# Kernel tuning notes

Hardware: AMD Instinct MI355X
Metric: run time of the kernel (lower is better)

## Reference

```python
import jax, jax.numpy as jnp
import numpy as np

B, C, N = 2, 128, 4096
BN_EPS = 1e-5


def setup_inputs() -> dict:
    key = jax.random.key(0)
    ks = jax.random.split(key, 16)
    Ch, Cd = C // 2, C // 8

    def bn_params(k1, c):
        k1, k2 = jax.random.split(k1)
        return (1.0 + 0.1 * jax.random.normal(k1, (c,), jnp.float32),  # gamma
                0.1 * jax.random.normal(k2, (c,), jnp.float32),        # beta
                jnp.zeros((c,), jnp.float32),                          # running mean
                jnp.ones((c,), jnp.float32))                           # running var

    g1, be1, m1, v1 = bn_params(ks[4], Ch)
    g2, be2, m2, v2 = bn_params(ks[5], Ch)
    gu, beu, mu, vu = bn_params(ks[6], C)
    return {
        "xyz": jax.random.normal(ks[0], (B, 3, N), jnp.float32),
        "features": jax.random.normal(ks[1], (B, C, N), jnp.float32),
        "w_mlp1": 0.1 * jax.random.normal(ks[2], (Ch, 6), jnp.float32),
        "b_mlp1": jnp.zeros((Ch,), jnp.float32),
        "g_mlp1": g1, "be_mlp1": be1, "m_mlp1": m1, "v_mlp1": v1,
        "w_mlp2": 0.05 * jax.random.normal(ks[3], (Ch, 2 * C), jnp.float32),
        "b_mlp2": jnp.zeros((Ch,), jnp.float32),
        "g_mlp2": g2, "be_mlp2": be2, "m_mlp2": m2, "v_mlp2": v2,
        "w_down1": 0.1 * jax.random.normal(ks[7], (Cd, C), jnp.float32),
        "w_down2": 0.1 * jax.random.normal(ks[8], (Cd, C), jnp.float32),
        "w_up": 0.1 * jax.random.normal(ks[9], (C, Cd), jnp.float32),
        "b_up": jnp.zeros((C,), jnp.float32),
        "g_up": gu, "be_up": beu, "m_up": mu, "v_up": vu,
        "k": 20,
    }


def _knn_idx(x, k):
    # x: [B,3,N]; pairwise_distance = -||xi-xj||^2, topk -> nearest
    xx = jnp.sum(x * x, axis=1)                       # [B,N]
    inner = jnp.einsum('bcn,bcm->bnm', x, x)          # [B,N,N]
    pd = 2.0 * inner - xx[:, :, None] - xx[:, None, :]
    return jax.lax.top_k(pd, k)[1]                    # [B,N,k]


def _gather_edge(feat_t, idx):
    # feat_t: [B,N,C], idx: [B,N,k] -> concat(nbr - center, center): [B,N,k,2C]
    nbr = jax.vmap(lambda a, i: a[i])(feat_t, idx)    # [B,N,k,C]
    center = feat_t[:, :, None, :]
    center_b = jnp.broadcast_to(center, nbr.shape)
    return jnp.concatenate((nbr - center, center_b), axis=-1)


def _bn(x, g, b, m, v, ch_axis=1):
    shape = [1] * x.ndim
    shape[ch_axis] = -1
    r = lambda p: p.reshape(shape)
    return (x - r(m)) * (r(g) / jnp.sqrt(r(v) + BN_EPS)) + r(b)


def reference(xyz, features, w_mlp1, b_mlp1, g_mlp1, be_mlp1, m_mlp1, v_mlp1,
              w_mlp2, b_mlp2, g_mlp2, be_mlp2, m_mlp2, v_mlp2,
              w_down1, w_down2, w_up, b_up, g_up, be_up, m_up, v_up, k):
    idx = _knn_idx(xyz, k)
    edge_x = _gather_edge(jnp.swapaxes(xyz, 1, 2), idx)        # [B,N,k,6]
    edge_f = _gather_edge(jnp.swapaxes(features, 1, 2), idx)   # [B,N,k,2C]

    # 1x1 conv2d + BN + ReLU on both branches (channels last via einsum)
    h1 = jnp.einsum('bnkc,oc->bonk', edge_x, w_mlp1) + b_mlp1[None, :, None, None]
    h1 = jax.nn.relu(_bn(h1, g_mlp1, be_mlp1, m_mlp1, v_mlp1))
    h2 = jnp.einsum('bnkc,oc->bonk', edge_f, w_mlp2) + b_mlp2[None, :, None, None]
    h2 = jax.nn.relu(_bn(h2, g_mlp2, be_mlp2, m_mlp2, v_mlp2))

    f_enc = jnp.max(jnp.concatenate((h1, h2), axis=1), axis=-1)  # [B,C,N]

    f1 = jax.nn.relu(jnp.einsum('bcn,oc->bon', f_enc, w_down1))  # [B,C/8,N]
    f2 = jax.nn.relu(jnp.einsum('bcn,oc->bon', f_enc, w_down2))

    # NOTE: original code indexes [0] after mean -> uses batch element 0 only
    f_channel = jnp.mean(f1, axis=-1, keepdims=True)[0]          # [C/8,1]
    f_space = jnp.mean(f2, axis=1, keepdims=True)[0]             # [1,N]
    final = jnp.sqrt(f_channel @ f_space + 1e-12)                # [C/8,N]
    final = final[None] + f1 + f2                                # [B,C/8,N]

    up = jnp.einsum('bcn,oc->bon', final, w_up) + b_up[None, :, None]
    final = jax.nn.relu(_bn(up, g_up, be_up, m_up, v_up))        # [B,C,N]

    f_local = f_enc - final
    return f_local * jnp.tanh(jax.nn.softplus(f_local))          # Mish
```

## Files before the change

kernel.cpp:

```cpp
#include <hip/hip_runtime.h>
#include <hip/hip_bf16.h>

#define BB 2
#define CC 128
#define NN 4096
#define KK 20

#define WS_FLAG   0
#define WS_FCACC  16
#define WS_S1     32
#define WS_C1     96
#define WS_S2     160
#define WS_C2     224
#define WS_SUP    288
#define WS_CUP    416
#define WS_FS     1024
#define WS_X      8192
#define WS_XX     32768
#define WS_W1     40960
#define WS_W2     41344
#define WS_WD1    57728
#define WS_WD2    59776
#define WS_WUP    61824
#define WS_P      65536
#define WS_Q      1114112
#define WS_FE     2326528
#define WS_F      WS_FE
#define WS_F12    3375104

struct InPtrs { const void* p[22]; };

__device__ __forceinline__ int detect_bf16(const void* xyz) {
  const unsigned* u = (const unsigned*)xyz;
  int cnt = 0;
  for (int i = 0; i < 64; ++i) {
    unsigned lo = u[i] & 0x7FFFu;
    cnt += (lo >= 0x3C00u && lo <= 0x4100u) ? 1 : 0;
  }
  return cnt >= 32;
}

__device__ __forceinline__ float ldin(const void* p, long long i, int flag) {
  if (flag) {
    unsigned short b = ((const unsigned short*)p)[i];
    return __uint_as_float(((unsigned)b) << 16);
  }
  return ((const float*)p)[i];
}

__device__ __forceinline__ double dkey(float v, int m) {
  unsigned u = __float_as_uint(v);
  u = (u & 0x80000000u) ? ~u : (u | 0x80000000u);
  return (double)u * 4096.0 + (double)((NN - 1) - m);
}

__device__ __forceinline__ void insert4d(double key,
    double& a0, double& a1, double& a2, double& a3) {
  bool b0 = key > a0, b1 = key > a1, b2 = key > a2, b3 = key > a3;
  a3 = b3 ? (b2 ? a2 : key) : a3;
  a2 = b2 ? (b1 ? a1 : key) : a2;
  a1 = b1 ? (b0 ? a0 : key) : a1;
  a0 = b0 ? key : a0;
}

__global__ __launch_bounds__(256) void k0_convert(InPtrs in, float* ws) {
  int flag = detect_bf16(in.p[0]);
  int gid = blockIdx.x * 256 + threadIdx.x;
  int stride = gridDim.x * 256;
  if (flag) {
    const ushort4* src = (const ushort4*)in.p[1];
    float4* dst = (float4*)(ws + WS_F);
    for (int i = gid; i < 262144; i += stride) {
      ushort4 s = src[i];
      dst[i] = make_float4(
        __uint_as_float(((unsigned)s.x) << 16), __uint_as_float(((unsigned)s.y) << 16),
        __uint_as_float(((unsigned)s.z) << 16), __uint_as_float(((unsigned)s.w) << 16));
    }
  } else {
    const float4* src = (const float4*)in.p[1];
    float4* dst = (float4*)(ws + WS_F);
    for (int i = gid; i < 262144; i += stride) dst[i] = src[i];
  }
  const int T0 = 24576;
  const int T1 = T0 + 384;
  const int T2 = T1 + 16384;
  const int T3 = T2 + 2048;
  const int T4 = T3 + 2048;
  const int T5 = T4 + 2048;
  for (int i = gid; i < T5; i += stride) {
    const void* src; int off, dst;
    if      (i < T0) { src = in.p[0];  off = i;      dst = WS_X   + off; }
    else if (i < T1) { src = in.p[2];  off = i - T0; dst = WS_W1  + off; }
    else if (i < T2) { src = in.p[8];  off = i - T1; dst = WS_W2  + off; }
    else if (i < T3) { src = in.p[14]; off = i - T2; dst = WS_WD1 + off; }
    else if (i < T4) { src = in.p[15]; off = i - T3; dst = WS_WD2 + off; }
    else             { src = in.p[16]; off = i - T4; dst = WS_WUP + off; }
    ws[dst] = ldin(src, off, flag);
  }
  if (blockIdx.x == 0) {
    int t = threadIdx.x;
    if (t < 64) {
      float b1 = ldin(in.p[3], t, flag), g1 = ldin(in.p[4], t, flag);
      float be1 = ldin(in.p[5], t, flag), m1 = ldin(in.p[6], t, flag), v1 = ldin(in.p[7], t, flag);
      float s1 = g1 / sqrtf(v1 + 1e-5f);
      ws[WS_S1 + t] = s1;
      ws[WS_C1 + t] = s1 * (b1 - m1) + be1;
      float b2 = ldin(in.p[9], t, flag), g2 = ldin(in.p[10], t, flag);
      float be2 = ldin(in.p[11], t, flag), m2 = ldin(in.p[12], t, flag), v2 = ldin(in.p[13], t, flag);
      float s2 = g2 / sqrtf(v2 + 1e-5f);
      ws[WS_S2 + t] = s2;
      ws[WS_C2 + t] = s2 * (b2 - m2) + be2;
    }
    if (t < 128) {
      float bu = ldin(in.p[17], t, flag), gu = ldin(in.p[18], t, flag);
      float beu = ldin(in.p[19], t, flag), mu = ldin(in.p[20], t, flag), vu = ldin(in.p[21], t, flag);
      float su = gu / sqrtf(vu + 1e-5f);
      ws[WS_SUP + t] = su;
      ws[WS_CUP + t] = su * (bu - mu) + beu;
    }
    if (t < 16) ws[WS_FCACC + t] = 0.f;
    if (t == 0) ((int*)ws)[WS_FLAG] = flag;
  }
}

__global__ __launch_bounds__(256) void k1_pq(float* ws) {
  __shared__ float ldsW[64 * 128];
  __shared__ float ldsF[64 * 32];
  int t = threadIdx.x;
  int bid = blockIdx.x;
  int b = bid >> 7;
  int m0 = (bid & 127) << 5;
  int w = t >> 6, sub = (t >> 5) & 1, mloc = t & 31;
  const float* F = ws + WS_F + (long long)b * CC * NN;
  const float* W2 = ws + WS_W2;
  float accP[8], accQ[8];
#pragma unroll
  for (int j = 0; j < 8; ++j) { accP[j] = 0.f; accQ[j] = 0.f; }
  for (int half = 0; half < 2; ++half) {
    if (half) __syncthreads();
    for (int i = t; i < 64 * 128; i += 256) {
      int o = i >> 7, r = i & 127;
      int c = (r & 63) + half * 64 + ((r >> 6) << 7);
      ldsW[i] = W2[o * 256 + c];
    }
    for (int i = t; i < 64 * 32; i += 256) {
      int cl = i >> 5, ml = i & 31;
      ldsF[i] = F[(long long)(half * 64 + cl) * NN + m0 + ml];
    }
    __syncthreads();
    for (int cl = 0; cl < 64; ++cl) {
      float f = ldsF[cl * 32 + mloc];
#pragma unroll
      for (int j = 0; j < 8; ++j) {
        int o = w * 16 + sub * 8 + j;
        accP[j] = fmaf(ldsW[o * 128 + cl], f, accP[j]);
        accQ[j] = fmaf(ldsW[o * 128 + 64 + cl], f, accQ[j]);
      }
    }
  }
  int m = m0 + mloc;
  const float* X = ws + WS_X + (long long)b * 3 * NN;
  float x0 = X[m], x1 = X[NN + m], x2 = X[2 * NN + m];
  const float* W1 = ws + WS_W1;
  float* P = ws + WS_P + ((long long)(b * NN + m)) * 128;
  float* Q = ws + WS_Q + ((long long)(b * NN + m)) * 128;
#pragma unroll
  for (int j = 0; j < 8; ++j) {
    int o = w * 16 + sub * 8 + j;
    float s1 = ws[WS_S1 + o], c1 = ws[WS_C1 + o];
    float px = fmaf(W1[o * 6 + 2], x2, fmaf(W1[o * 6 + 1], x1, W1[o * 6 + 0] * x0));
    float qx = fmaf(W1[o * 6 + 5], x2, fmaf(W1[o * 6 + 4], x1, W1[o * 6 + 3] * x0));
    P[o] = s1 * px;
    Q[o] = fmaf(s1, qx - px, c1);
    float s2 = ws[WS_S2 + o], c2 = ws[WS_C2 + o];
    P[64 + o] = s2 * accP[j];
    Q[64 + o] = fmaf(s2, accQ[j] - accP[j], c2);
  }
  if (t < 32) {
    float xx = __fadd_rn(__fadd_rn(__fmul_rn(x0, x0), __fmul_rn(x1, x1)), __fmul_rn(x2, x2));
    ws[WS_XX + b * NN + m] = xx;
  }
}

__global__ __launch_bounds__(256) void k23_knn_fenc(float* ws) {
  int t = threadIdx.x;
  int w = t >> 6, lane = t & 63;
  int pt = blockIdx.x * 4 + w;
  int b = pt >> 12;
  int n = pt & (NN - 1);
  const float* X = ws + WS_X + (long long)b * 3 * NN;
  const float* XX = ws + WS_XX + (long long)b * NN;
  float xc0 = X[n], xc1 = X[NN + n], xc2 = X[2 * NN + n], xxn = XX[n];
  double a0 = -1.0, a1 = -1.0, a2 = -1.0, a3 = -1.0;
#pragma unroll 4
  for (int s = 0; s < 64; ++s) {
    int m = s * 64 + lane;
    float c0 = X[m], c1 = X[NN + m], c2 = X[2 * NN + m], xxm = XX[m];
    float inner = __fadd_rn(__fadd_rn(__fmul_rn(c0, xc0), __fmul_rn(c1, xc1)), __fmul_rn(c2, xc2));
    float pd = __fsub_rn(__fsub_rn(__fmul_rn(2.0f, inner), xxn), xxm);
    insert4d(dkey(pd, m), a0, a1, a2, a3);
  }
  unsigned long long used = 0;
  int nv = 4;
  double winner = 0.0;
  for (int r = 0; r < KK; ++r) {
    double v = a0;
#pragma unroll
    for (int off = 1; off < 64; off <<= 1)
      v = fmax(v, __shfl_xor(v, off));
    if (lane == r) winner = v;
    if (a0 == v) {
      unsigned hi = (unsigned)(v * (1.0 / 4096.0));
      double rem = v - 4096.0 * (double)hi;
      int mm = (NN - 1) - (int)rem;
      used |= 1ull << (mm >> 6);
      a0 = a1; a1 = a2; a2 = a3; a3 = -1.0; --nv;
      if (nv == 0) {
        a0 = a1 = a2 = a3 = -1.0;
#pragma unroll 1
        for (int s = 0; s < 64; ++s) {
          if (!((used >> s) & 1ull)) {
            int m = s * 64 + lane;
            float c0 = X[m], c1 = X[NN + m], c2 = X[2 * NN + m], xxm = XX[m];
            float inner = __fadd_rn(__fadd_rn(__fmul_rn(c0, xc0), __fmul_rn(c1, xc1)), __fmul_rn(c2, xc2));
            float pd = __fsub_rn(__fsub_rn(__fmul_rn(2.0f, inner), xxn), xxm);
            insert4d(dkey(pd, m), a0, a1, a2, a3);
          }
        }
        nv = 4;
      }
    }
  }
  int myidx;
  {
    unsigned hi = (unsigned)(winner * (1.0 / 4096.0));
    double rem = winner - 4096.0 * (double)hi;
    myidx = (NN - 1) - (int)rem;
  }
  const float* Q = ws + WS_Q + (long long)pt * 128;
  const float* Pb = ws + WS_P + (long long)b * NN * 128;
  float2 q = ((const float2*)Q)[lane];
  float mx0 = -3.4e38f, mx1 = -3.4e38f;
#pragma unroll
  for (int j = 0; j < KK; ++j) {
    int id = __shfl(myidx, j);
    float2 p = ((const float2*)(Pb + (long long)id * 128))[lane];
    mx0 = fmaxf(mx0, p.x + q.x);
    mx1 = fmaxf(mx1, p.y + q.y);
  }
  float2 fe = make_float2(fmaxf(mx0, 0.f), fmaxf(mx1, 0.f));
  ((float2*)(ws + WS_FE + (long long)pt * 128))[lane] = fe;
}

__global__ __launch_bounds__(256) void k4_down(float* ws) {
  __shared__ float ldsFE[8 * 128];
  __shared__ float ldsW[32 * 129];
  __shared__ float ldsFC[16];
  int t = threadIdx.x;
  int b = blockIdx.x >> 9;
  int n0 = (blockIdx.x & 511) << 3;
  for (int i = t; i < 8 * 128; i += 256) {
    int p = i >> 7, c = i & 127;
    ldsFE[i] = ws[WS_FE + (long long)(b * NN + n0 + p) * 128 + c];
  }
  for (int i = t; i < 32 * 128; i += 256) {
    int o = i >> 7, c = i & 127;
    ldsW[o * 129 + c] = (o < 16) ? ws[WS_WD1 + o * 128 + c] : ws[WS_WD2 + (o - 16) * 128 + c];
  }
  if (t < 16) ldsFC[t] = 0.f;
  __syncthreads();
  int p = t >> 5, oid = t & 31;
  float acc = 0.f;
#pragma unroll 8
  for (int c = 0; c < 128; ++c)
    acc = fmaf(ldsW[oid * 129 + c], ldsFE[p * 128 + c], acc);
  float v = fmaxf(acc, 0.f);
  ws[WS_F12 + (long long)(b * NN + n0 + p) * 32 + oid] = v;
  if (b == 0) {
    if (oid >= 16) {
      float s = v;
#pragma unroll
      for (int d = 1; d < 16; d <<= 1) s += __shfl_xor(s, d);
      if (oid == 16) ws[WS_FS + n0 + p] = s * 0.0625f;
    } else {
      atomicAdd(&ldsFC[oid], v);
    }
  }
  __syncthreads();
  if (b == 0 && t < 16) atomicAdd(ws + WS_FCACC + t, ldsFC[t]);
}

__global__ __launch_bounds__(256) void k5_final(float* ws, float* outf, __hip_bfloat16* outb) {
  __shared__ float fin[16 * 16];
  int t = threadIdx.x;
  int g = t >> 4;
  int p = t & 15;
  int b = blockIdx.x >> 8;
  int n0 = (blockIdx.x & 255) << 4;
  int n = n0 + p;
  int flag = ((const int*)ws)[WS_FLAG];
  {
    float fs = ws[WS_FS + n];
    float fc = ws[WS_FCACC + g] * (1.0f / NN);
    float f1v = ws[WS_F12 + (long long)(b * NN + n) * 32 + g];
    float f2v = ws[WS_F12 + (long long)(b * NN + n) * 32 + 16 + g];
    fin[p * 16 + g] = sqrtf(fc * fs + 1e-12f) + f1v + f2v;
  }
  __syncthreads();
  const float4* FE4 = (const float4*)(ws + WS_FE + (long long)(b * NN + n) * 128 + g * 8);
  float fev[8];
  {
    float4 a = FE4[0], c = FE4[1];
    fev[0] = a.x; fev[1] = a.y; fev[2] = a.z; fev[3] = a.w;
    fev[4] = c.x; fev[5] = c.y; fev[6] = c.z; fev[7] = c.w;
  }
#pragma unroll
  for (int j = 0; j < 8; ++j) {
    int o = g * 8 + j;
    float acc = 0.f;
#pragma unroll
    for (int c = 0; c < 16; ++c)
      acc = fmaf(ws[WS_WUP + o * 16 + c], fin[p * 16 + c], acc);
    float fo = fmaf(ws[WS_SUP + o], acc, ws[WS_CUP + o]);
    fo = fmaxf(fo, 0.f);
    float fl = fev[j] - fo;
    float u = __expf(fl);
    float nmr = u * (u + 2.f);
    float y = fl * __fdividef(nmr, nmr + 2.f);
    if (fl > 15.f) y = fl;
    long long oi = ((long long)b * CC + o) * NN + n;
    if (flag) outb[oi] = __float2bfloat16(y);
    else      outf[oi] = y;
  }
}

extern "C" void kernel_launch(void* const* d_in, const int* in_sizes, int n_in,
                              void* d_out, int out_size, void* d_ws, size_t ws_size,
                              hipStream_t stream) {
  (void)in_sizes; (void)out_size; (void)ws_size;
  float* ws = (float*)d_ws;
  InPtrs ip;
  for (int i = 0; i < 22; ++i) ip.p[i] = (i < n_in) ? d_in[i] : nullptr;
  hipLaunchKernelGGL(k0_convert,   dim3(512),          dim3(256), 0, stream, ip, ws);
  hipLaunchKernelGGL(k1_pq,        dim3(256),          dim3(256), 0, stream, ws);
  hipLaunchKernelGGL(k23_knn_fenc, dim3(BB * NN / 4),  dim3(256), 0, stream, ws);
  hipLaunchKernelGGL(k4_down,      dim3(BB * NN / 8),  dim3(256), 0, stream, ws);
  hipLaunchKernelGGL(k5_final,     dim3(BB * NN / 16), dim3(256), 0, stream, ws,
                     (float*)d_out, (__hip_bfloat16*)d_out);
}
```

Measured before the change: 224.2 us.

## Fuse input conversion into consumers and merge down-projection into KNN kernel

```diff
diff --git a/kernel.cpp b/kernel.cpp
--- a/kernel.cpp
+++ b/kernel.cpp
@@ -6,26 +6,13 @@
 #define NN 4096
 #define KK 20
 
-#define WS_FLAG   0
 #define WS_FCACC  16
-#define WS_S1     32
-#define WS_C1     96
-#define WS_S2     160
-#define WS_C2     224
-#define WS_SUP    288
-#define WS_CUP    416
 #define WS_FS     1024
 #define WS_X      8192
 #define WS_XX     32768
-#define WS_W1     40960
-#define WS_W2     41344
-#define WS_WD1    57728
-#define WS_WD2    59776
-#define WS_WUP    61824
 #define WS_P      65536
 #define WS_Q      1114112
 #define WS_FE     2326528
-#define WS_F      WS_FE
 #define WS_F12    3375104
 
 struct InPtrs { const void* p[22]; };
@@ -63,76 +50,46 @@
   a0 = b0 ? key : a0;
 }
 
-__global__ __launch_bounds__(256) void k0_convert(InPtrs in, float* ws) {
-  int flag = detect_bf16(in.p[0]);
-  int gid = blockIdx.x * 256 + threadIdx.x;
-  int stride = gridDim.x * 256;
-  if (flag) {
-    const ushort4* src = (const ushort4*)in.p[1];
-    float4* dst = (float4*)(ws + WS_F);
-    for (int i = gid; i < 262144; i += stride) {
-      ushort4 s = src[i];
-      dst[i] = make_float4(
-        __uint_as_float(((unsigned)s.x) << 16), __uint_as_float(((unsigned)s.y) << 16),
-        __uint_as_float(((unsigned)s.z) << 16), __uint_as_float(((unsigned)s.w) << 16));
-    }
-  } else {
-    const float4* src = (const float4*)in.p[1];
-    float4* dst = (float4*)(ws + WS_F);
-    for (int i = gid; i < 262144; i += stride) dst[i] = src[i];
-  }
-  const int T0 = 24576;
-  const int T1 = T0 + 384;
-  const int T2 = T1 + 16384;
-  const int T3 = T2 + 2048;
-  const int T4 = T3 + 2048;
-  const int T5 = T4 + 2048;
-  for (int i = gid; i < T5; i += stride) {
-    const void* src; int off, dst;
-    if      (i < T0) { src = in.p[0];  off = i;      dst = WS_X   + off; }
-    else if (i < T1) { src = in.p[2];  off = i - T0; dst = WS_W1  + off; }
-    else if (i < T2) { src = in.p[8];  off = i - T1; dst = WS_W2  + off; }
-    else if (i < T3) { src = in.p[14]; off = i - T2; dst = WS_WD1 + off; }
-    else if (i < T4) { src = in.p[15]; off = i - T3; dst = WS_WD2 + off; }
-    else             { src = in.p[16]; off = i - T4; dst = WS_WUP + off; }
-    ws[dst] = ldin(src, off, flag);
-  }
-  if (blockIdx.x == 0) {
-    int t = threadIdx.x;
-    if (t < 64) {
-      float b1 = ldin(in.p[3], t, flag), g1 = ldin(in.p[4], t, flag);
-      float be1 = ldin(in.p[5], t, flag), m1 = ldin(in.p[6], t, flag), v1 = ldin(in.p[7], t, flag);
-      float s1 = g1 / sqrtf(v1 + 1e-5f);
-      ws[WS_S1 + t] = s1;
-      ws[WS_C1 + t] = s1 * (b1 - m1) + be1;
-      float b2 = ldin(in.p[9], t, flag), g2 = ldin(in.p[10], t, flag);
-      float be2 = ldin(in.p[11], t, flag), m2 = ldin(in.p[12], t, flag), v2 = ldin(in.p[13], t, flag);
-      float s2 = g2 / sqrtf(v2 + 1e-5f);
-      ws[WS_S2 + t] = s2;
-      ws[WS_C2 + t] = s2 * (b2 - m2) + be2;
-    }
-    if (t < 128) {
-      float bu = ldin(in.p[17], t, flag), gu = ldin(in.p[18], t, flag);
-      float beu = ldin(in.p[19], t, flag), mu = ldin(in.p[20], t, flag), vu = ldin(in.p[21], t, flag);
-      float su = gu / sqrtf(vu + 1e-5f);
-      ws[WS_SUP + t] = su;
-      ws[WS_CUP + t] = su * (bu - mu) + beu;
-    }
-    if (t < 16) ws[WS_FCACC + t] = 0.f;
-    if (t == 0) ((int*)ws)[WS_FLAG] = flag;
-  }
-}
-
-__global__ __launch_bounds__(256) void k1_pq(float* ws) {
+__global__ __launch_bounds__(256) void k1_pq(InPtrs in, float* ws) {
   __shared__ float ldsW[64 * 128];
   __shared__ float ldsF[64 * 32];
+  __shared__ float sS1[64], sC1[64], sS2[64], sC2[64], sW1[384];
+  int flag = detect_bf16(in.p[0]);
   int t = threadIdx.x;
   int bid = blockIdx.x;
+  {
+    int gid = bid * 256 + t;
+    if (gid < BB * NN) {
+      int b = gid >> 12, m = gid & (NN - 1);
+      long long xb = (long long)b * 3 * NN;
+      float x0 = ldin(in.p[0], xb + m, flag);
+      float x1 = ldin(in.p[0], xb + NN + m, flag);
+      float x2 = ldin(in.p[0], xb + 2 * NN + m, flag);
+      ws[WS_X + xb + m] = x0;
+      ws[WS_X + xb + NN + m] = x1;
+      ws[WS_X + xb + 2 * NN + m] = x2;
+      ws[WS_XX + gid] =
+        __fadd_rn(__fadd_rn(__fmul_rn(x0, x0), __fmul_rn(x1, x1)), __fmul_rn(x2, x2));
+    }
+    if (bid == 0 && t < 16) ws[WS_FCACC + t] = 0.f;
+  }
+  if (t < 64) {
+    float g1 = ldin(in.p[4], t, flag), v1 = ldin(in.p[7], t, flag);
+    float s1 = g1 / sqrtf(v1 + 1e-5f);
+    float b1 = ldin(in.p[3], t, flag), be1 = ldin(in.p[5], t, flag), m1v = ldin(in.p[6], t, flag);
+    sS1[t] = s1; sC1[t] = s1 * (b1 - m1v) + be1;
+    float g2 = ldin(in.p[10], t, flag), v2 = ldin(in.p[13], t, flag);
+    float s2 = g2 / sqrtf(v2 + 1e-5f);
+    float b2 = ldin(in.p[9], t, flag), be2 = ldin(in.p[11], t, flag), m2v = ldin(in.p[12], t, flag);
+    sS2[t] = s2; sC2[t] = s2 * (b2 - m2v) + be2;
+  }
+  for (int i = t; i < 384; i += 256) sW1[i] = ldin(in.p[2], i, flag);
   int b = bid >> 7;
   int m0 = (bid & 127) << 5;
   int w = t >> 6, sub = (t >> 5) & 1, mloc = t & 31;
-  const float* F = ws + WS_F + (long long)b * CC * NN;
-  const float* W2 = ws + WS_W2;
+  const void* Fin = in.p[1];
+  const void* W2in = in.p[8];
+  long long fb = (long long)b * CC * NN;
   float accP[8], accQ[8];
 #pragma unroll
   for (int j = 0; j < 8; ++j) { accP[j] = 0.f; accQ[j] = 0.f; }
@@ -141,11 +98,11 @@
     for (int i = t; i < 64 * 128; i += 256) {
       int o = i >> 7, r = i & 127;
       int c = (r & 63) + half * 64 + ((r >> 6) << 7);
-      ldsW[i] = W2[o * 256 + c];
+      ldsW[i] = ldin(W2in, o * 256 + c, flag);
     }
     for (int i = t; i < 64 * 32; i += 256) {
       int cl = i >> 5, ml = i & 31;
-      ldsF[i] = F[(long long)(half * 64 + cl) * NN + m0 + ml];
+      ldsF[i] = ldin(Fin, fb + (long long)(half * 64 + cl) * NN + m0 + ml, flag);
     }
     __syncthreads();
     for (int cl = 0; cl < 64; ++cl) {
@@ -159,35 +116,42 @@
     }
   }
   int m = m0 + mloc;
-  const float* X = ws + WS_X + (long long)b * 3 * NN;
-  float x0 = X[m], x1 = X[NN + m], x2 = X[2 * NN + m];
-  const float* W1 = ws + WS_W1;
+  long long xb = (long long)b * 3 * NN;
+  float x0 = ldin(in.p[0], xb + m, flag);
+  float x1 = ldin(in.p[0], xb + NN + m, flag);
+  float x2 = ldin(in.p[0], xb + 2 * NN + m, flag);
   float* P = ws + WS_P + ((long long)(b * NN + m)) * 128;
   float* Q = ws + WS_Q + ((long long)(b * NN + m)) * 128;
 #pragma unroll
   for (int j = 0; j < 8; ++j) {
     int o = w * 16 + sub * 8 + j;
-    float s1 = ws[WS_S1 + o], c1 = ws[WS_C1 + o];
-    float px = fmaf(W1[o * 6 + 2], x2, fmaf(W1[o * 6 + 1], x1, W1[o * 6 + 0] * x0));
-    float qx = fmaf(W1[o * 6 + 5], x2, fmaf(W1[o * 6 + 4], x1, W1[o * 6 + 3] * x0));
+    float s1 = sS1[o], c1 = sC1[o];
+    float px = fmaf(sW1[o * 6 + 2], x2, fmaf(sW1[o * 6 + 1], x1, sW1[o * 6 + 0] * x0));
+    float qx = fmaf(sW1[o * 6 + 5], x2, fmaf(sW1[o * 6 + 4], x1, sW1[o * 6 + 3] * x0));
     P[o] = s1 * px;
     Q[o] = fmaf(s1, qx - px, c1);
-    float s2 = ws[WS_S2 + o], c2 = ws[WS_C2 + o];
+    float s2 = sS2[o], c2 = sC2[o];
     P[64 + o] = s2 * accP[j];
     Q[64 + o] = fmaf(s2, accQ[j] - accP[j], c2);
   }
-  if (t < 32) {
-    float xx = __fadd_rn(__fadd_rn(__fmul_rn(x0, x0), __fmul_rn(x1, x1)), __fmul_rn(x2, x2));
-    ws[WS_XX + b * NN + m] = xx;
-  }
-}
-
-__global__ __launch_bounds__(256) void k23_knn_fenc(float* ws) {
+}
+
+__global__ __launch_bounds__(256) void k23_knn_fenc_down(InPtrs in, float* ws) {
+  __shared__ float ldsW[32 * 129];
+  __shared__ float ldsFE[4 * 128];
+  __shared__ float ldsFC[16];
+  int flag = detect_bf16(in.p[0]);
   int t = threadIdx.x;
   int w = t >> 6, lane = t & 63;
   int pt = blockIdx.x * 4 + w;
   int b = pt >> 12;
   int n = pt & (NN - 1);
+  for (int i = t; i < 32 * 128; i += 256) {
+    int o = i >> 7, c = i & 127;
+    ldsW[o * 129 + c] = (o < 16) ? ldin(in.p[14], o * 128 + c, flag)
+                                 : ldin(in.p[15], (o - 16) * 128 + c, flag);
+  }
+  if (t < 16) ldsFC[t] = 0.f;
   const float* X = ws + WS_X + (long long)b * 3 * NN;
   const float* XX = ws + WS_XX + (long long)b * NN;
   float xc0 = X[n], xc1 = X[NN + n], xc2 = X[2 * NN + n], xxn = XX[n];
@@ -250,55 +214,48 @@
   }
   float2 fe = make_float2(fmaxf(mx0, 0.f), fmaxf(mx1, 0.f));
   ((float2*)(ws + WS_FE + (long long)pt * 128))[lane] = fe;
-}
-
-__global__ __launch_bounds__(256) void k4_down(float* ws) {
-  __shared__ float ldsFE[8 * 128];
-  __shared__ float ldsW[32 * 129];
-  __shared__ float ldsFC[16];
-  int t = threadIdx.x;
-  int b = blockIdx.x >> 9;
-  int n0 = (blockIdx.x & 511) << 3;
-  for (int i = t; i < 8 * 128; i += 256) {
-    int p = i >> 7, c = i & 127;
-    ldsFE[i] = ws[WS_FE + (long long)(b * NN + n0 + p) * 128 + c];
-  }
-  for (int i = t; i < 32 * 128; i += 256) {
-    int o = i >> 7, c = i & 127;
-    ldsW[o * 129 + c] = (o < 16) ? ws[WS_WD1 + o * 128 + c] : ws[WS_WD2 + (o - 16) * 128 + c];
-  }
-  if (t < 16) ldsFC[t] = 0.f;
+  ((float2*)(ldsFE + w * 128))[lane] = fe;
   __syncthreads();
-  int p = t >> 5, oid = t & 31;
+  int oid = lane & 31, hf = lane >> 5;
   float acc = 0.f;
 #pragma unroll 8
-  for (int c = 0; c < 128; ++c)
-    acc = fmaf(ldsW[oid * 129 + c], ldsFE[p * 128 + c], acc);
+  for (int cl = 0; cl < 64; ++cl)
+    acc = fmaf(ldsW[oid * 129 + hf * 64 + cl], ldsFE[w * 128 + hf * 64 + cl], acc);
+  acc += __shfl_xor(acc, 32);
   float v = fmaxf(acc, 0.f);
-  ws[WS_F12 + (long long)(b * NN + n0 + p) * 32 + oid] = v;
+  if (hf == 0) ws[WS_F12 + (long long)pt * 32 + oid] = v;
   if (b == 0) {
-    if (oid >= 16) {
+    if (hf == 1 && oid >= 16) {
       float s = v;
 #pragma unroll
       for (int d = 1; d < 16; d <<= 1) s += __shfl_xor(s, d);
-      if (oid == 16) ws[WS_FS + n0 + p] = s * 0.0625f;
-    } else {
-      atomicAdd(&ldsFC[oid], v);
-    }
+      if (oid == 16) ws[WS_FS + n] = s * 0.0625f;
+    }
+    if (hf == 0 && oid < 16) atomicAdd(&ldsFC[oid], v);
   }
   __syncthreads();
   if (b == 0 && t < 16) atomicAdd(ws + WS_FCACC + t, ldsFC[t]);
 }
 
-__global__ __launch_bounds__(256) void k5_final(float* ws, float* outf, __hip_bfloat16* outb) {
+__global__ __launch_bounds__(256) void k5_final(InPtrs in, float* ws,
+                                                float* outf, __hip_bfloat16* outb) {
   __shared__ float fin[16 * 16];
+  __shared__ float sWUP[2048];
+  __shared__ float sSU[128], sCU[128];
+  int flag = detect_bf16(in.p[0]);
   int t = threadIdx.x;
   int g = t >> 4;
   int p = t & 15;
   int b = blockIdx.x >> 8;
   int n0 = (blockIdx.x & 255) << 4;
   int n = n0 + p;
-  int flag = ((const int*)ws)[WS_FLAG];
+  for (int i = t; i < 2048; i += 256) sWUP[i] = ldin(in.p[16], i, flag);
+  if (t < 128) {
+    float gu = ldin(in.p[18], t, flag), vu = ldin(in.p[21], t, flag);
+    float su = gu / sqrtf(vu + 1e-5f);
+    float bu = ldin(in.p[17], t, flag), beu = ldin(in.p[19], t, flag), mu = ldin(in.p[20], t, flag);
+    sSU[t] = su; sCU[t] = su * (bu - mu) + beu;
+  }
   {
     float fs = ws[WS_FS + n];
     float fc = ws[WS_FCACC + g] * (1.0f / NN);
@@ -320,8 +277,8 @@
     float acc = 0.f;
 #pragma unroll
     for (int c = 0; c < 16; ++c)
-      acc = fmaf(ws[WS_WUP + o * 16 + c], fin[p * 16 + c], acc);
-    float fo = fmaf(ws[WS_SUP + o], acc, ws[WS_CUP + o]);
+      acc = fmaf(sWUP[o * 16 + c], fin[p * 16 + c], acc);
+    float fo = fmaf(sSU[o], acc, sCU[o]);
     fo = fmaxf(fo, 0.f);
     float fl = fev[j] - fo;
     float u = __expf(fl);
@@ -341,10 +298,8 @@
   float* ws = (float*)d_ws;
   InPtrs ip;
   for (int i = 0; i < 22; ++i) ip.p[i] = (i < n_in) ? d_in[i] : nullptr;
-  hipLaunchKernelGGL(k0_convert,   dim3(512),          dim3(256), 0, stream, ip, ws);
-  hipLaunchKernelGGL(k1_pq,        dim3(256),          dim3(256), 0, stream, ws);
-  hipLaunchKernelGGL(k23_knn_fenc, dim3(BB * NN / 4),  dim3(256), 0, stream, ws);
-  hipLaunchKernelGGL(k4_down,      dim3(BB * NN / 8),  dim3(256), 0, stream, ws);
-  hipLaunchKernelGGL(k5_final,     dim3(BB * NN / 16), dim3(256), 0, stream, ws,
+  hipLaunchKernelGGL(k1_pq,              dim3(256),          dim3(256), 0, stream, ip, ws);
+  hipLaunchKernelGGL(k23_knn_fenc_down,  dim3(BB * NN / 4),  dim3(256), 0, stream, ip, ws);
+  hipLaunchKernelGGL(k5_final,           dim3(BB * NN / 16), dim3(256), 0, stream, ip, ws,
                      (float*)d_out, (__hip_bfloat16*)d_out);
 }
```

Measured after the change: 233.1 us. 4.0% more time.
